# Performance work log

Hardware: AMD Instinct MI355X
Metric: run time of the kernel (lower is better)

## Reference

```python
import jax, jax.numpy as jnp
import numpy as np

D_EMBED = 64      # per-head dim (module uses d_embed as head dim)
N_HEADS = 8
SCALE = 1.0 / float(np.sqrt(D_EMBED))
ROPE_BASE = 10000.0


def _rope(x):
    # torchtune-style interleaved RoPE. x: [B, S, H, D]
    B, S, H, D = x.shape
    freqs = 1.0 / (ROPE_BASE ** (jnp.arange(0, D, 2, dtype=jnp.float32) / D))  # [D/2]
    ang = jnp.arange(S, dtype=jnp.float32)[:, None] * freqs[None, :]           # [S, D/2]
    cos = jnp.cos(ang)[None, :, None, :]
    sin = jnp.sin(ang)[None, :, None, :]
    x1 = x[..., 0::2]
    x2 = x[..., 1::2]
    return jnp.stack([x1 * cos - x2 * sin, x1 * sin + x2 * cos], axis=-1).reshape(B, S, H, D)


def setup_inputs() -> dict:
    key = jax.random.key(0)
    ks = jax.random.split(key, 5)
    B, S, D, H = 2, 2048, D_EMBED, N_HEADS
    std = 1.0 / np.sqrt(D)
    return {
        "q": jax.random.normal(ks[0], (B, S, D), jnp.float32),
        "Wq": jax.random.normal(ks[1], (H * D, D), jnp.float32) * std,
        "Wk": jax.random.normal(ks[2], (H * D, D), jnp.float32) * std,
        "Wv": jax.random.normal(ks[3], (H * D, D), jnp.float32) * std,
        "Wo": jax.random.normal(ks[4], (D, H * D), jnp.float32) * std,
        "gamma": jnp.ones((H,), jnp.float32),
    }


def reference(q, Wq, Wk, Wv, Wo, gamma):
    B, S, D = q.shape
    H = N_HEADS
    qh = (q @ Wq.T).reshape(B, S, H, D)
    kh = (q @ Wk.T).reshape(B, S, H, D)
    vh = (q @ Wv.T).reshape(B, S, H, D)
    qh = _rope(qh).transpose(0, 2, 1, 3)  # [B,H,S,D]
    kh = _rope(kh).transpose(0, 2, 1, 3)
    vh = vh.transpose(0, 2, 1, 3)
    # RBF attention scores
    qn = jnp.sum(qh * qh, axis=-1, keepdims=True)                 # [B,H,S,1]
    kn = jnp.sum(kh * kh, axis=-1, keepdims=True)                 # [B,H,S,1]
    qk = jnp.einsum('bhsd,bhtd->bhst', qh, kh)                    # [B,H,S,S]
    dist = jnp.maximum(qn - 2.0 * qk + jnp.swapaxes(kn, -2, -1), 0.0)
    scores = jnp.exp(-(gamma[None, :, None, None] * SCALE) * dist)
    causal = jnp.tril(jnp.ones((S, S), dtype=bool))
    scores = jnp.where(causal, scores, 0.0)
    out = jnp.einsum('bhst,bhtd->bhsd', scores, vh)
    out = out.transpose(0, 2, 1, 3).reshape(B, S, H * D)
    return out @ Wo.T
```

## Files before the change

### kernel.cpp

```cpp
#include <hip/hip_runtime.h>
#include <hip/hip_bf16.h>

#define BB 2
#define SS 2048
#define DD 64
#define HH 8
#define HD 512
#define SCALE 0.125f

typedef __bf16 bf16;
typedef __attribute__((ext_vector_type(4))) __bf16 bf16x4;
typedef __attribute__((ext_vector_type(8))) __bf16 bf16x8;
typedef __attribute__((ext_vector_type(4))) float floatx4;

#define PSLOT 2097152

__device__ __forceinline__ floatx4 mfma16(bf16x8 a, bf16x8 b, floatx4 c) {
    return __builtin_amdgcn_mfma_f32_16x16x32_bf16(a, b, c, 0, 0, 0);
}

#define PV_MFMA(ACC, A, B) \
    asm("s_nop 1\n\tv_mfma_f32_16x16x16_bf16 %0, %1, %2, %0" \
        : "+v"(ACC) : "v"(A), "v"(B))

#define MFMA_DRAIN4(A0, A1, A2, A3) \
    asm volatile("s_nop 7\n\ts_nop 7" : "+v"(A0), "+v"(A1), "+v"(A2), "+v"(A3))

#define GLL(G, L) __builtin_amdgcn_global_load_lds( \
    (const __attribute__((address_space(1))) void*)(G), \
    (__attribute__((address_space(3))) void*)(L), 16, 0, 0)

__device__ __forceinline__ bf16x8 load8(const void* base, size_t idx, int f32) {
    if (f32) {
        const float* p = (const float*)base + idx;
        const float4 a = *reinterpret_cast<const float4*>(p);
        const float4 b = *reinterpret_cast<const float4*>(p + 4);
        bf16x8 r;
        r[0] = (bf16)a.x; r[1] = (bf16)a.y; r[2] = (bf16)a.z; r[3] = (bf16)a.w;
        r[4] = (bf16)b.x; r[5] = (bf16)b.y; r[6] = (bf16)b.z; r[7] = (bf16)b.w;
        return r;
    }
    return *reinterpret_cast<const bf16x8*>((const bf16*)base + idx);
}

__device__ __forceinline__ float load1(const void* base, int idx, int f32) {
    return f32 ? ((const float*)base)[idx] : (float)((const bf16*)base)[idx];
}

__global__ __launch_bounds__(256) void proj_rope_kernel(
    const void* __restrict__ q, const void* __restrict__ Wq,
    const void* __restrict__ Wk, const void* __restrict__ Wv,
    const void* __restrict__ gamma,
    bf16* __restrict__ qh, bf16* __restrict__ kh, bf16* __restrict__ vt,
    float* __restrict__ qn, float* __restrict__ kn,
    int* __restrict__ flagw)
{
    const int lane = threadIdx.x & 63;
    const int wid  = blockIdx.x * 4 + (threadIdx.x >> 6);
    if (wid >= 3 * BB * HH * (SS / 64)) return;
    const int l16  = lane & 15;
    const int quad = lane >> 4;

    int hit = 0;
    const unsigned short* qu = (const unsigned short*)q;
#pragma unroll
    for (int i = 0; i < 16; ++i) {
        const unsigned short u = qu[lane + i * 64];
        if (((u >> 7) & 0xFF) >= 134) hit = 1;
    }
    const int f32 = (__ballot(hit) != 0ull) ? 1 : 0;
    if (wid == 0 && lane == 0) *flagw = f32;

    int id = wid;
    const int h   = id % HH; id /= HH;
    const int st4 = id % (SS / 64); id /= (SS / 64);
    const int b   = id % BB; id /= BB;
    const int w   = id;

    const void* W = (w == 0) ? Wq : (w == 1) ? Wk : Wv;
    const size_t bh = (size_t)b * HH + h;

    bf16x8 wb0[4], wb1[4];
#pragma unroll
    for (int t = 0; t < 4; ++t) {
        const size_t wrow = (size_t)(h * 64 + t * 16 + l16) * DD;
        wb0[t] = load8(W, wrow + quad * 8, f32);
        wb1[t] = load8(W, wrow + quad * 8 + 32, f32);
    }

    float frevA[4], frevB[4];
    float ncc = 0.f;
    if (w < 2) {
        ncc = -load1(gamma, h, f32) * SCALE * 1.4426950408889634f;
#pragma unroll
        for (int t = 0; t < 4; ++t) {
            const int dbase = t * 16 + quad * 4;
            frevA[t] = __builtin_amdgcn_exp2f(
                -(float)dbase * (13.2877123795f / 64.0f)) * 0.15915494309f;
            frevB[t] = __builtin_amdgcn_exp2f(
                -(float)(dbase + 2) * (13.2877123795f / 64.0f)) * 0.15915494309f;
        }
    }

    for (int s4 = 0; s4 < 4; ++s4) {
        const int s0 = (st4 * 4 + s4) * 16;
        const size_t qrow = ((size_t)b * SS + s0 + l16) * DD;
        bf16x8 a0 = load8(q, qrow + quad * 8, f32);
        bf16x8 a1 = load8(q, qrow + quad * 8 + 32, f32);

        floatx4 cv[4];
#pragma unroll
        for (int t = 0; t < 4; ++t) {
            floatx4 acc = {0.f, 0.f, 0.f, 0.f};
            if (w < 2) {
                acc = mfma16(wb0[t], a0, acc);
                acc = mfma16(wb1[t], a1, acc);
            } else {
                acc = mfma16(a0, wb0[t], acc);
                acc = mfma16(a1, wb1[t], acc);
            }
            cv[t] = acc;
        }

        if (w < 2) {
            bf16*  dst  = (w == 0) ? qh : kh;
            float* ndst = (w == 0) ? qn : kn;
            const float srowf = (float)(s0 + l16);
            float nacc = 0.f;
            bf16* drow = dst + (bh * SS + s0 + l16) * DD + quad * 4;
#pragma unroll
            for (int t = 0; t < 4; ++t) {
                float revA = srowf * frevA[t]; revA -= floorf(revA);
                float revB = srowf * frevB[t]; revB -= floorf(revB);
                const float snA = __builtin_amdgcn_sinf(revA);
                const float csA = __builtin_amdgcn_cosf(revA);
                const float snB = __builtin_amdgcn_sinf(revB);
                const float csB = __builtin_amdgcn_cosf(revB);
                const float x0 = cv[t][0], x1 = cv[t][1];
                const float x2 = cv[t][2], x3 = cv[t][3];
                const float r0 = x0 * csA - x1 * snA;
                const float r1 = x0 * snA + x1 * csA;
                const float r2 = x2 * csB - x3 * snB;
                const float r3 = x2 * snB + x3 * csB;
                nacc += r0 * r0 + r1 * r1 + r2 * r2 + r3 * r3;
                bf16x4 o; o[0]=(bf16)r0; o[1]=(bf16)r1; o[2]=(bf16)r2; o[3]=(bf16)r3;
                *reinterpret_cast<bf16x4*>(drow + t * 16) = o;
            }
            nacc += __shfl_xor(nacc, 16);
            nacc += __shfl_xor(nacc, 32);
            if (quad == 0) ndst[bh * SS + s0 + l16] = ncc * nacc;
        } else {
            bf16* vrow = vt + ((size_t)bh * 128 + st4 * 4 + s4) * 1024
                       + l16 * 16 + quad * 4;
#pragma unroll
            for (int t = 0; t < 4; ++t) {
                bf16x4 pv;
#pragma unroll
                for (int r = 0; r < 4; ++r) pv[r] = (bf16)cv[t][r];
                *reinterpret_cast<bf16x4*>(vrow + t * 256) = pv;
            }
        }
    }
}

__global__ __launch_bounds__(256) void attn_kernel(
    const bf16* __restrict__ qh, const bf16* __restrict__ kh,
    const bf16* __restrict__ vt, const float* __restrict__ qn,
    const float* __restrict__ kn, const void* __restrict__ gamma,
    bf16* __restrict__ partial, const int* __restrict__ flagp,
    int NU, int U, int pb)
{
    __shared__ __align__(16) char smem[16384];
    const int f32  = *flagp;
    const int tid  = threadIdx.x;
    const int wv   = tid >> 6;
    const int lane = tid & 63;
    const int l16  = lane & 15;
    const int quad = lane >> 4;

    const int xcd  = blockIdx.x & 7;
    int sblk = blockIdx.x >> 3;
    const int half = (sblk >= pb) ? 1 : 0;
    const int bh   = xcd + (half << 3);
    sblk -= half * pb;

    const int j   = sblk / NU;
    const int u   = sblk - j * NU;
    const int B   = 2 * (j + 1);
    const int c0  = u * U;
    const int nA  = (c0 < B) ? (((c0 + U) < B ? (c0 + U) : B) - c0) : 0;
    const int bB  = ((c0 > B ? c0 : B) - B);
    const int slotA = u;
    const int slotB = u - (B / U);
    const int h    = bh & 7;

    const float twocc = 2.0f * load1(gamma, h, f32) * SCALE * 1.4426950408889634f;

    int q4 = (nA > 0) ? j : (31 - j);
    int s0 = (q4 * 4 + wv) * 16;

    const bf16* qb = qh + ((size_t)bh * SS + s0 + l16) * DD;
    bf16x8 aq0 = *reinterpret_cast<const bf16x8*>(qb + quad * 8);
    bf16x8 aq1 = *reinterpret_cast<const bf16x8*>(qb + quad * 8 + 32);
    float qnc_l = qn[(size_t)bh * SS + s0 + l16];

    floatx4 acc0 = {0.f,0.f,0.f,0.f}, acc1 = {0.f,0.f,0.f,0.f};
    floatx4 acc2 = {0.f,0.f,0.f,0.f}, acc3 = {0.f,0.f,0.f,0.f};

    const float* knp   = kn + (size_t)bh * SS + quad * 4;
    const char* kgbase = (const char*)(kh + (size_t)bh * SS * DD);
    const char* vgbase = (const char*)(vt + (size_t)bh * 131072);

    const int jK   = wv * 64 + lane;
    const int keyK = jK >> 3;
    const int cK   = ((jK & 7) - keyK) & 7;
    const int goffK = keyK * 128 + cK * 16;
    const int goffV = jK * 16;
    char* ldsK = smem + wv * 1024;
    char* ldsV = smem + 8192 + wv * 1024;

    const int kro0 = (l16 * 8 + ((quad + l16) & 7)) * 16;
    const int kro1 = (l16 * 8 + ((quad + 4 + l16) & 7)) * 16;
    const int vro  = l16 * 32 + quad * 8;

#define T0_OF(C) (((C) < nA ? (c0 + (C)) : (bB + (C) - nA)) * 32)

#define STORE_O(SLOT, S0) do { \
    bf16* pbp = partial + (size_t)(SLOT) * PSLOT \
              + ((size_t)bh * SS + (S0) + l16) * DD + quad * 4; \
    bf16x4 o_; \
    o_[0]=(bf16)acc0[0]; o_[1]=(bf16)acc0[1]; o_[2]=(bf16)acc0[2]; o_[3]=(bf16)acc0[3]; \
    *reinterpret_cast<bf16x4*>(pbp +  0) = o_; \
    o_[0]=(bf16)acc1[0]; o_[1]=(bf16)acc1[1]; o_[2]=(bf16)acc1[2]; o_[3]=(bf16)acc1[3]; \
    *reinterpret_cast<bf16x4*>(pbp + 16) = o_; \
    o_[0]=(bf16)acc2[0]; o_[1]=(bf16)acc2[1]; o_[2]=(bf16)acc2[2]; o_[3]=(bf16)acc2[3]; \
    *reinterpret_cast<bf16x4*>(pbp + 32) = o_; \
    o_[0]=(bf16)acc3[0]; o_[1]=(bf16)acc3[1]; o_[2]=(bf16)acc3[2]; o_[3]=(bf16)acc3[3]; \
    *reinterpret_cast<bf16x4*>(pbp + 48) = o_; \
} while (0)

    {
        const int t0p = T0_OF(0);
        GLL(kgbase + (size_t)t0p * 128 + goffK, ldsK);
        GLL(vgbase + (size_t)(t0p >> 4) * 2048 + goffV, ldsV);
    }

    int buf = 0;
    for (int c = 0; c < U; ++c) {
        __builtin_amdgcn_s_barrier();

        const int t0 = T0_OF(c);
        const float4 knv0 = *reinterpret_cast<const float4*>(knp + t0);
        const float4 knv1 = *reinterpret_cast<const float4*>(knp + t0 + 16);

        if (c == nA && nA > 0) {
            MFMA_DRAIN4(acc0, acc1, acc2, acc3);
            STORE_O(slotA, s0);
            acc0 = {0.f,0.f,0.f,0.f}; acc1 = {0.f,0.f,0.f,0.f};
            acc2 = {0.f,0.f,0.f,0.f}; acc3 = {0.f,0.f,0.f,0.f};
            q4 = 31 - j;
            s0 = (q4 * 4 + wv) * 16;
            const bf16* qb2 = qh + ((size_t)bh * SS + s0 + l16) * DD;
            aq0 = *reinterpret_cast<const bf16x8*>(qb2 + quad * 8);
            aq1 = *reinterpret_cast<const bf16x8*>(qb2 + quad * 8 + 32);
            qnc_l = qn[(size_t)bh * SS + s0 + l16];
        }

        asm volatile("" ::: "memory");

        const int tn = T0_OF((c + 1 < U) ? (c + 1) : c);
        GLL(kgbase + (size_t)tn * 128 + goffK, ldsK + ((buf ^ 1) << 12));
        GLL(vgbase + (size_t)(tn >> 4) * 2048 + goffV, ldsV + ((buf ^ 1) << 12));

        asm volatile("s_waitcnt vmcnt(4)" ::: "memory");

        const char* Kb = smem + (buf << 12);
        const char* Vb = smem + 8192 + (buf << 12);

        bf16x8 kc0 = *reinterpret_cast<const bf16x8*>(Kb + kro0);
        bf16x8 kc1 = *reinterpret_cast<const bf16x8*>(Kb + kro1);
        bf16x8 kc2 = *reinterpret_cast<const bf16x8*>(Kb + 2048 + kro0);
        bf16x8 kc3 = *reinterpret_cast<const bf16x8*>(Kb + 2048 + kro1);
        bf16x4 v00 = *reinterpret_cast<const bf16x4*>(Vb + vro);
        bf16x4 v01 = *reinterpret_cast<const bf16x4*>(Vb + 512 + vro);
        bf16x4 v02 = *reinterpret_cast<const bf16x4*>(Vb + 1024 + vro);
        bf16x4 v03 = *reinterpret_cast<const bf16x4*>(Vb + 1536 + vro);
        bf16x4 v10 = *reinterpret_cast<const bf16x4*>(Vb + 2048 + vro);
        bf16x4 v11 = *reinterpret_cast<const bf16x4*>(Vb + 2560 + vro);
        bf16x4 v12 = *reinterpret_cast<const bf16x4*>(Vb + 3072 + vro);
        bf16x4 v13 = *reinterpret_cast<const bf16x4*>(Vb + 3584 + vro);

        floatx4 z0 = {0.f,0.f,0.f,0.f};
        z0 = mfma16(kc0, aq0, z0);
        z0 = mfma16(kc1, aq1, z0);
        floatx4 z1 = {0.f,0.f,0.f,0.f};
        z1 = mfma16(kc2, aq0, z1);
        z1 = mfma16(kc3, aq1, z1);

        const float* k0_ = (const float*)&knv0;
        const float* k1_ = (const float*)&knv1;
        bf16x4 p0, p1;
        if (t0 + 31 <= s0) {
#pragma unroll
            for (int i = 0; i < 4; ++i) {
                float rawA = fmaf(twocc, z0[i], qnc_l + k0_[i]);
                float rawB = fmaf(twocc, z1[i], qnc_l + k1_[i]);
                p0[i] = (bf16)__builtin_amdgcn_exp2f(rawA);
                p1[i] = (bf16)__builtin_amdgcn_exp2f(rawB);
            }
        } else {
            const int dq0 = s0 + l16 - t0 - quad * 4;
            const int dq1 = dq0 - 16;
#pragma unroll
            for (int i = 0; i < 4; ++i) {
                float rawA = fmaf(twocc, z0[i], qnc_l + k0_[i]);
                float rawB = fmaf(twocc, z1[i], qnc_l + k1_[i]);
                float eA = __builtin_amdgcn_exp2f(rawA);
                float eB = __builtin_amdgcn_exp2f(rawB);
                p0[i] = (bf16)((i <= dq0) ? eA : 0.f);
                p1[i] = (bf16)((i <= dq1) ? eB : 0.f);
            }
        }

        PV_MFMA(acc0, v00, p0);
        PV_MFMA(acc1, v01, p0);
        PV_MFMA(acc2, v02, p0);
        PV_MFMA(acc3, v03, p0);
        PV_MFMA(acc0, v10, p1);
        PV_MFMA(acc1, v11, p1);
        PV_MFMA(acc2, v12, p1);
        PV_MFMA(acc3, v13, p1);

        buf ^= 1;
    }

    MFMA_DRAIN4(acc0, acc1, acc2, acc3);
    STORE_O((nA == U) ? slotA : slotB, s0);
#undef STORE_O
#undef T0_OF
}

template <int NACT>
__device__ __forceinline__ floatx4 opj_core(const bf16* __restrict__ partial,
                                            const void* __restrict__ Wo,
                                            int b, int srow, size_t brow,
                                            int f32, int quad) {
    floatx4 acc = {0.f, 0.f, 0.f, 0.f};
#pragma unroll 4
    for (int kk = 0; kk < HD; kk += 32) {
        const int h  = kk >> 6;
        const int d0 = (kk & 63) + quad * 8;
        const bf16* ap = partial + (((size_t)(b * 8 + h)) * SS + srow) * 64 + d0;
        bf16x8 v0 = *reinterpret_cast<const bf16x8*>(ap);
        float u[8];
#pragma unroll
        for (int i = 0; i < 8; ++i) u[i] = (float)v0[i];
#pragma unroll
        for (int s = 1; s < NACT; ++s) {
            bf16x8 vs = *reinterpret_cast<const bf16x8*>(ap + (size_t)s * PSLOT);
#pragma unroll
            for (int i = 0; i < 8; ++i) u[i] += (float)vs[i];
        }
        bf16x8 a;
#pragma unroll
        for (int i = 0; i < 8; ++i) a[i] = (bf16)u[i];
        bf16x8 w = load8(Wo, brow + kk, f32);
        acc = mfma16(a, w, acc);
    }
    return acc;
}

__global__ __launch_bounds__(256) void outproj_kernel(
    const bf16* __restrict__ partial, const void* __restrict__ Wo,
    void* __restrict__ out, const int* __restrict__ flagp, int NU, int U)
{
    const int f32  = *flagp;
    const int ct   = threadIdx.x >> 6;
    const int lane = threadIdx.x & 63;
    const int l16  = lane & 15;
    const int quad = lane >> 4;

    const int g0   = blockIdx.x * 16;
    const int b    = g0 >> 11;
    const int s0   = g0 & (SS - 1);
    const int srow = s0 + l16;
    const size_t brow = (size_t)(ct * 16 + l16) * HD + quad * 8;

    const int q4g = s0 >> 6;
    int nact;
    if (q4g < 16) { const int Bp = 2 * (q4g + 1); nact = (Bp + U - 1) / U; }
    else          { const int Bp = 2 * (32 - q4g); nact = NU - Bp / U; }

    floatx4 acc;
    switch (nact) {
        case 1:  acc = opj_core<1>(partial, Wo, b, srow, brow, f32, quad); break;
        case 2:  acc = opj_core<2>(partial, Wo, b, srow, brow, f32, quad); break;
        case 3:  acc = opj_core<3>(partial, Wo, b, srow, brow, f32, quad); break;
        default: acc = opj_core<4>(partial, Wo, b, srow, brow, f32, quad); break;
    }

#pragma unroll
    for (int r = 0; r < 4; ++r) {
        const size_t o = (size_t)(g0 + quad * 4 + r) * DD + ct * 16 + l16;
        if (f32) ((float*)out)[o] = acc[r];
        else     ((bf16*)out)[o]  = (bf16)acc[r];
    }
}

extern "C" void kernel_launch(void* const* d_in, const int* in_sizes, int n_in,
                              void* d_out, int out_size, void* d_ws, size_t ws_size,
                              hipStream_t stream) {
    const void* q     = d_in[0];
    const void* Wq    = d_in[1];
    const void* Wk    = d_in[2];
    const void* Wv    = d_in[3];
    const void* Wo    = d_in[4];
    const void* gamma = d_in[5];

    char* ws = (char*)d_ws;
    bf16*  qh      = (bf16*)(ws);
    bf16*  kh      = (bf16*)(ws + 4194304);
    bf16*  vt      = (bf16*)(ws + 8388608);
    float* qn      = (float*)(ws + 12582912);
    float* kn      = (float*)(ws + 12713984);
    int*   flag    = (int*)  (ws + 12845056);
    bf16*  partial = (bf16*)(ws + 13631488);

    const size_t base = 13631488ull;
    int NU = (ws_size >= base + 3ull * 4194304) ? 3 : 2;
    const int U  = 66 / NU;
    const int pb = 16 * NU;

    const int nproj = 3 * BB * HH * (SS / 64);
    proj_rope_kernel<<<dim3((nproj + 3) / 4), dim3(256), 0, stream>>>(
        q, Wq, Wk, Wv, gamma, qh, kh, vt, qn, kn, flag);
    attn_kernel<<<dim3(16 * pb), dim3(256), 0, stream>>>(
        qh, kh, vt, qn, kn, gamma, partial, flag, NU, U, pb);
    outproj_kernel<<<dim3(BB * SS / 16), dim3(256), 0, stream>>>(
        partial, Wo, d_out, flag, NU, U);
}
```

Baseline: 115.3 us.

## Replace LDS-staged K/V pipeline with register double-buffered direct global loads

The attention kernel no longer stages K and V tiles through shared memory via global_load_lds with per-iteration barriers. Each wave now loads its K, V and key-norm fragments straight from global memory into registers, double-buffering two fragment sets (A/B) in a loop unrolled by two. This removes the LDS round trip, the shared-memory allocation and the block-wide barriers. In exchange each wave issues its own global loads without sharing across waves, which raises register pressure and global/L2 traffic.

```diff
diff --git a/kernel.cpp b/kernel.cpp
--- a/kernel.cpp
+++ b/kernel.cpp
@@ -25,10 +25,6 @@
 
 #define MFMA_DRAIN4(A0, A1, A2, A3) \
     asm volatile("s_nop 7\n\ts_nop 7" : "+v"(A0), "+v"(A1), "+v"(A2), "+v"(A3))
-
-#define GLL(G, L) __builtin_amdgcn_global_load_lds( \
-    (const __attribute__((address_space(1))) void*)(G), \
-    (__attribute__((address_space(3))) void*)(L), 16, 0, 0)
 
 __device__ __forceinline__ bf16x8 load8(const void* base, size_t idx, int f32) {
     if (f32) {
@@ -170,7 +166,6 @@
     bf16* __restrict__ partial, const int* __restrict__ flagp,
     int NU, int U, int pb)
 {
-    __shared__ __align__(16) char smem[16384];
     const int f32  = *flagp;
     const int tid  = threadIdx.x;
     const int wv   = tid >> 6;
@@ -208,20 +203,9 @@
     floatx4 acc2 = {0.f,0.f,0.f,0.f}, acc3 = {0.f,0.f,0.f,0.f};
 
     const float* knp   = kn + (size_t)bh * SS + quad * 4;
-    const char* kgbase = (const char*)(kh + (size_t)bh * SS * DD);
+    const bf16* khb    = kh + (size_t)bh * SS * DD;
     const char* vgbase = (const char*)(vt + (size_t)bh * 131072);
-
-    const int jK   = wv * 64 + lane;
-    const int keyK = jK >> 3;
-    const int cK   = ((jK & 7) - keyK) & 7;
-    const int goffK = keyK * 128 + cK * 16;
-    const int goffV = jK * 16;
-    char* ldsK = smem + wv * 1024;
-    char* ldsV = smem + 8192 + wv * 1024;
-
-    const int kro0 = (l16 * 8 + ((quad + l16) & 7)) * 16;
-    const int kro1 = (l16 * 8 + ((quad + 4 + l16) & 7)) * 16;
-    const int vro  = l16 * 32 + quad * 8;
+    const int   vro    = l16 * 32 + quad * 8;
 
 #define T0_OF(C) (((C) < nA ? (c0 + (C)) : (bB + (C) - nA)) * 32)
 
@@ -239,103 +223,107 @@
     *reinterpret_cast<bf16x4*>(pbp + 48) = o_; \
 } while (0)
 
-    {
-        const int t0p = T0_OF(0);
-        GLL(kgbase + (size_t)t0p * 128 + goffK, ldsK);
-        GLL(vgbase + (size_t)(t0p >> 4) * 2048 + goffV, ldsV);
-    }
-
-    int buf = 0;
-    for (int c = 0; c < U; ++c) {
-        __builtin_amdgcn_s_barrier();
-
-        const int t0 = T0_OF(c);
-        const float4 knv0 = *reinterpret_cast<const float4*>(knp + t0);
-        const float4 knv1 = *reinterpret_cast<const float4*>(knp + t0 + 16);
-
-        if (c == nA && nA > 0) {
-            MFMA_DRAIN4(acc0, acc1, acc2, acc3);
-            STORE_O(slotA, s0);
-            acc0 = {0.f,0.f,0.f,0.f}; acc1 = {0.f,0.f,0.f,0.f};
-            acc2 = {0.f,0.f,0.f,0.f}; acc3 = {0.f,0.f,0.f,0.f};
-            q4 = 31 - j;
-            s0 = (q4 * 4 + wv) * 16;
-            const bf16* qb2 = qh + ((size_t)bh * SS + s0 + l16) * DD;
-            aq0 = *reinterpret_cast<const bf16x8*>(qb2 + quad * 8);
-            aq1 = *reinterpret_cast<const bf16x8*>(qb2 + quad * 8 + 32);
-            qnc_l = qn[(size_t)bh * SS + s0 + l16];
+#define DECL_FRAGS(S) \
+    bf16x8 kc0##S, kc1##S, kc2##S, kc3##S; \
+    bf16x4 v00##S, v01##S, v02##S, v03##S, v10##S, v11##S, v12##S, v13##S; \
+    float4 knv0##S, knv1##S;
+
+#define LOAD_FRAGS(S, T0C) do { \
+    const int t0l = (T0C); \
+    const bf16* kr = khb + ((size_t)t0l + l16) * DD + quad * 8; \
+    kc0##S = *reinterpret_cast<const bf16x8*>(kr); \
+    kc1##S = *reinterpret_cast<const bf16x8*>(kr + 32); \
+    kc2##S = *reinterpret_cast<const bf16x8*>(kr + 1024); \
+    kc3##S = *reinterpret_cast<const bf16x8*>(kr + 1056); \
+    const char* vb = vgbase + (size_t)(t0l >> 4) * 2048 + vro; \
+    v00##S = *reinterpret_cast<const bf16x4*>(vb); \
+    v01##S = *reinterpret_cast<const bf16x4*>(vb + 512); \
+    v02##S = *reinterpret_cast<const bf16x4*>(vb + 1024); \
+    v03##S = *reinterpret_cast<const bf16x4*>(vb + 1536); \
+    v10##S = *reinterpret_cast<const bf16x4*>(vb + 2048); \
+    v11##S = *reinterpret_cast<const bf16x4*>(vb + 2560); \
+    v12##S = *reinterpret_cast<const bf16x4*>(vb + 3072); \
+    v13##S = *reinterpret_cast<const bf16x4*>(vb + 3584); \
+    knv0##S = *reinterpret_cast<const float4*>(knp + t0l); \
+    knv1##S = *reinterpret_cast<const float4*>(knp + t0l + 16); \
+} while (0)
+
+#define BOUNDARY(C) do { if ((C) == nA && nA > 0) { \
+    MFMA_DRAIN4(acc0, acc1, acc2, acc3); \
+    STORE_O(slotA, s0); \
+    acc0 = {0.f,0.f,0.f,0.f}; acc1 = {0.f,0.f,0.f,0.f}; \
+    acc2 = {0.f,0.f,0.f,0.f}; acc3 = {0.f,0.f,0.f,0.f}; \
+    q4 = 31 - j; \
+    s0 = (q4 * 4 + wv) * 16; \
+    const bf16* qb2 = qh + ((size_t)bh * SS + s0 + l16) * DD; \
+    aq0 = *reinterpret_cast<const bf16x8*>(qb2 + quad * 8); \
+    aq1 = *reinterpret_cast<const bf16x8*>(qb2 + quad * 8 + 32); \
+    qnc_l = qn[(size_t)bh * SS + s0 + l16]; \
+} } while (0)
+
+#define COMPUTE(S, T0C) do { \
+    const int t0c = (T0C); \
+    floatx4 z0 = {0.f,0.f,0.f,0.f}; \
+    z0 = mfma16(kc0##S, aq0, z0); \
+    z0 = mfma16(kc1##S, aq1, z0); \
+    floatx4 z1 = {0.f,0.f,0.f,0.f}; \
+    z1 = mfma16(kc2##S, aq0, z1); \
+    z1 = mfma16(kc3##S, aq1, z1); \
+    const float* k0_ = (const float*)&knv0##S; \
+    const float* k1_ = (const float*)&knv1##S; \
+    bf16x4 p0, p1; \
+    if (t0c + 31 <= s0) { \
+        _Pragma("unroll") \
+        for (int i = 0; i < 4; ++i) { \
+            float rawA = fmaf(twocc, z0[i], qnc_l + k0_[i]); \
+            float rawB = fmaf(twocc, z1[i], qnc_l + k1_[i]); \
+            p0[i] = (bf16)__builtin_amdgcn_exp2f(rawA); \
+            p1[i] = (bf16)__builtin_amdgcn_exp2f(rawB); \
+        } \
+    } else { \
+        const int dq0 = s0 + l16 - t0c - quad * 4; \
+        const int dq1 = dq0 - 16; \
+        _Pragma("unroll") \
+        for (int i = 0; i < 4; ++i) { \
+            float rawA = fmaf(twocc, z0[i], qnc_l + k0_[i]); \
+            float rawB = fmaf(twocc, z1[i], qnc_l + k1_[i]); \
+            float eA = __builtin_amdgcn_exp2f(rawA); \
+            float eB = __builtin_amdgcn_exp2f(rawB); \
+            p0[i] = (bf16)((i <= dq0) ? eA : 0.f); \
+            p1[i] = (bf16)((i <= dq1) ? eB : 0.f); \
+        } \
+    } \
+    PV_MFMA(acc0, v00##S, p0); \
+    PV_MFMA(acc1, v01##S, p0); \
+    PV_MFMA(acc2, v02##S, p0); \
+    PV_MFMA(acc3, v03##S, p0); \
+    PV_MFMA(acc0, v10##S, p1); \
+    PV_MFMA(acc1, v11##S, p1); \
+    PV_MFMA(acc2, v12##S, p1); \
+    PV_MFMA(acc3, v13##S, p1); \
+} while (0)
+
+    DECL_FRAGS(A)
+    DECL_FRAGS(B)
+
+    LOAD_FRAGS(A, T0_OF(0));
+    for (int c = 0; c < U; c += 2) {
+        if (c + 1 < U) LOAD_FRAGS(B, T0_OF(c + 1));
+        BOUNDARY(c);
+        COMPUTE(A, T0_OF(c));
+        if (c + 2 < U) LOAD_FRAGS(A, T0_OF(c + 2));
+        if (c + 1 < U) {
+            BOUNDARY(c + 1);
+            COMPUTE(B, T0_OF(c + 1));
         }
-
-        asm volatile("" ::: "memory");
-
-        const int tn = T0_OF((c + 1 < U) ? (c + 1) : c);
-        GLL(kgbase + (size_t)tn * 128 + goffK, ldsK + ((buf ^ 1) << 12));
-        GLL(vgbase + (size_t)(tn >> 4) * 2048 + goffV, ldsV + ((buf ^ 1) << 12));
-
-        asm volatile("s_waitcnt vmcnt(4)" ::: "memory");
-
-        const char* Kb = smem + (buf << 12);
-        const char* Vb = smem + 8192 + (buf << 12);
-
-        bf16x8 kc0 = *reinterpret_cast<const bf16x8*>(Kb + kro0);
-        bf16x8 kc1 = *reinterpret_cast<const bf16x8*>(Kb + kro1);
-        bf16x8 kc2 = *reinterpret_cast<const bf16x8*>(Kb + 2048 + kro0);
-        bf16x8 kc3 = *reinterpret_cast<const bf16x8*>(Kb + 2048 + kro1);
-        bf16x4 v00 = *reinterpret_cast<const bf16x4*>(Vb + vro);
-        bf16x4 v01 = *reinterpret_cast<const bf16x4*>(Vb + 512 + vro);
-        bf16x4 v02 = *reinterpret_cast<const bf16x4*>(Vb + 1024 + vro);
-        bf16x4 v03 = *reinterpret_cast<const bf16x4*>(Vb + 1536 + vro);
-        bf16x4 v10 = *reinterpret_cast<const bf16x4*>(Vb + 2048 + vro);
-        bf16x4 v11 = *reinterpret_cast<const bf16x4*>(Vb + 2560 + vro);
-        bf16x4 v12 = *reinterpret_cast<const bf16x4*>(Vb + 3072 + vro);
-        bf16x4 v13 = *reinterpret_cast<const bf16x4*>(Vb + 3584 + vro);
-
-        floatx4 z0 = {0.f,0.f,0.f,0.f};
-        z0 = mfma16(kc0, aq0, z0);
-        z0 = mfma16(kc1, aq1, z0);
-        floatx4 z1 = {0.f,0.f,0.f,0.f};
-        z1 = mfma16(kc2, aq0, z1);
-        z1 = mfma16(kc3, aq1, z1);
-
-        const float* k0_ = (const float*)&knv0;
-        const float* k1_ = (const float*)&knv1;
-        bf16x4 p0, p1;
-        if (t0 + 31 <= s0) {
-#pragma unroll
-            for (int i = 0; i < 4; ++i) {
-                float rawA = fmaf(twocc, z0[i], qnc_l + k0_[i]);
-                float rawB = fmaf(twocc, z1[i], qnc_l + k1_[i]);
-                p0[i] = (bf16)__builtin_amdgcn_exp2f(rawA);
-                p1[i] = (bf16)__builtin_amdgcn_exp2f(rawB);
-            }
-        } else {
-            const int dq0 = s0 + l16 - t0 - quad * 4;
-            const int dq1 = dq0 - 16;
-#pragma unroll
-            for (int i = 0; i < 4; ++i) {
-                float rawA = fmaf(twocc, z0[i], qnc_l + k0_[i]);
-                float rawB = fmaf(twocc, z1[i], qnc_l + k1_[i]);
-                float eA = __builtin_amdgcn_exp2f(rawA);
-                float eB = __builtin_amdgcn_exp2f(rawB);
-                p0[i] = (bf16)((i <= dq0) ? eA : 0.f);
-                p1[i] = (bf16)((i <= dq1) ? eB : 0.f);
-            }
-        }
-
-        PV_MFMA(acc0, v00, p0);
-        PV_MFMA(acc1, v01, p0);
-        PV_MFMA(acc2, v02, p0);
-        PV_MFMA(acc3, v03, p0);
-        PV_MFMA(acc0, v10, p1);
-        PV_MFMA(acc1, v11, p1);
-        PV_MFMA(acc2, v12, p1);
-        PV_MFMA(acc3, v13, p1);
-
-        buf ^= 1;
     }
 
     MFMA_DRAIN4(acc0, acc1, acc2, acc3);
     STORE_O((nA == U) ? slotA : slotB, s0);
+#undef COMPUTE
+#undef BOUNDARY
+#undef LOAD_FRAGS
+#undef DECL_FRAGS
 #undef STORE_O
 #undef T0_OF
 }
```

New measurement: 144.0 us. 1.25x slower.
